# Kernel tuning notes

Hardware: AMD Instinct MI355X
Metric: run time of the kernel (lower is better)

## Reference

```python
import jax, jax.numpy as jnp
import numpy as np

B, S, HID, H = 2, 2048, 1024, 16
D_HEAD = HID // H  # 64
EPS = 1e-5


def _gammas():
    lo, hi = np.log(1.0 / 512.0), np.log(1.0 / 32.0)
    return (1.0 - np.exp(np.linspace(lo, hi, H))).astype(np.float32)


def _decay_mask():
    # D[h, n, m] = gamma_h^(n-m) for n >= m else 0  (causal exponential decay)
    gam = jnp.asarray(_gammas())                      # [H]
    pos = jnp.arange(S, dtype=jnp.float32)
    diff = pos[:, None] - pos[None, :]                # [S, S]
    keep = diff >= 0
    logg = jnp.log(gam)[:, None, None]                # [H,1,1]
    safe = jnp.where(keep, diff, 0.0)[None]           # avoid inf for masked entries
    return jnp.where(keep[None], jnp.exp(safe * logg), 0.0)  # [H, S, S]


def setup_inputs() -> dict:
    key = jax.random.key(0)
    ks = jax.random.split(key, 10)
    rn = lambda k, shape, s=1.0: jax.random.normal(k, shape, dtype=jnp.float32) * s
    return {
        "x": rn(ks[0], (B, S, HID)),
        "wq": rn(ks[1], (H, D_HEAD, D_HEAD), 1.0 / np.sqrt(D_HEAD)),
        "bq": rn(ks[2], (H, D_HEAD), 0.02),
        "wk": rn(ks[3], (H, D_HEAD, D_HEAD), 1.0 / np.sqrt(D_HEAD)),
        "bk": rn(ks[4], (H, D_HEAD), 0.02),
        "wv": rn(ks[5], (H, D_HEAD, D_HEAD), 1.0 / np.sqrt(D_HEAD)),
        "theta": rn(ks[6], (H, D_HEAD), 1.0 / D_HEAD),
        "gn_weight": jnp.ones((HID,), jnp.float32),
        "gn_bias": jnp.zeros((HID,), jnp.float32),
        "weight1": rn(ks[7], (HID, HID), 1.0 / HID),
        "weight2": rn(ks[8], (HID, HID), 1.0 / HID),
    }


def reference(x, wq, bq, wk, bk, wv, theta, gn_weight, gn_bias, weight1, weight2):
    # Per-head retention (all heads vectorized; torch loops over heads).
    xh = x.reshape(B, S, H, D_HEAD)
    q = jnp.einsum('bshd,hde->bshe', xh, wq) + bq
    k = jnp.einsum('bshd,hde->bshe', xh, wk) + bk
    v = jnp.einsum('bshd,hde->bshe', xh, wv)
    # Complex rotary factors exp(i*n*theta) on q, conj on k -> real part of q k^H:
    ang = jnp.arange(S, dtype=jnp.float32)[:, None, None] * theta[None]  # [S,H,d]
    cs, sn = jnp.cos(ang), jnp.sin(ang)
    scores = (jnp.einsum('bshd,bthd->bhst', q * cs, k * cs)
              + jnp.einsum('bshd,bthd->bhst', q * sn, k * sn))  # Re(QK^H) [B,H,S,S]
    scores = scores * _decay_mask()[None]                        # decay mask
    ret = jnp.einsum('bhst,bthd->bshd', scores, v)               # [B,S,H,d]
    # GroupNorm with groups = n_heads over channels (per-head normalization).
    mean = jnp.mean(ret, axis=-1, keepdims=True)
    var = jnp.var(ret, axis=-1, keepdims=True)
    retn = (ret - mean) * jax.lax.rsqrt(var + EPS)
    retn = retn.reshape(B, S, HID) * gn_weight + gn_bias
    # Swish gate on x @ W1, residual add, project with W2.
    gate = x @ weight1
    out = gate * jax.nn.sigmoid(gate) + retn
    return out @ weight2
```

## Files before the change

kernel.cpp:

```cpp
#include <hip/hip_runtime.h>
#include <cstdint>
#include <cstddef>

#define B_ 2
#define S_ 2048
#define HID_ 1024
#define H_ 16
#define DH_ 64

typedef __attribute__((ext_vector_type(8))) short short8;
typedef __attribute__((ext_vector_type(8))) unsigned short ushort8;
typedef __attribute__((ext_vector_type(4))) unsigned short ushort4v;
typedef __attribute__((ext_vector_type(4))) float floatx4;
typedef __attribute__((ext_vector_type(4))) float float4v;

static __device__ __forceinline__ unsigned short f2bf(float f) {
  unsigned int u = __float_as_uint(f);
  u += 0x7fffu + ((u >> 16) & 1u);
  return (unsigned short)(u >> 16);
}
static __device__ __forceinline__ float bf2f(unsigned short h) {
  return __uint_as_float(((unsigned int)h) << 16);
}

__global__ __launch_bounds__(256) void convert_kernel(
    const float* __restrict__ x, const float* __restrict__ w1,
    const float* __restrict__ w2, unsigned short* __restrict__ x_bf,
    unsigned short* __restrict__ w1t, unsigned short* __restrict__ w2t_hi,
    unsigned short* __restrict__ w2t_lo) {
  const int NX = B_ * S_ * HID_;
  const int NW = HID_ * HID_;
  int idx = blockIdx.x * 256 + threadIdx.x;
  if (idx < NX) {
    x_bf[idx] = f2bf(x[idx]);
  } else if (idx < NX + NW) {
    int i = idx - NX;
    int n = i >> 10, k = i & 1023;
    w1t[i] = f2bf(w1[k * HID_ + n]);
  } else if (idx < NX + 2 * NW) {
    int i = idx - NX - NW;
    int n = i >> 10, k = i & 1023;
    float v = w2[k * HID_ + n];
    unsigned short h = f2bf(v);
    w2t_hi[i] = h;
    w2t_lo[i] = f2bf(v - bf2f(h));
  }
}

__global__ __launch_bounds__(256) void qkv_kernel(
    const float* __restrict__ x, const float* __restrict__ wq,
    const float* __restrict__ bq, const float* __restrict__ wk,
    const float* __restrict__ bk, const float* __restrict__ wv,
    const float* __restrict__ theta,
    unsigned short* __restrict__ q_h, unsigned short* __restrict__ q_l,
    unsigned short* __restrict__ k_h, unsigned short* __restrict__ k_l,
    unsigned short* __restrict__ v_th, unsigned short* __restrict__ v_tl,
    int b) {
  __shared__ __align__(16) float xs[64 * 68];
  __shared__ __align__(16) float wqs[64 * 68];
  __shared__ __align__(16) float wks[64 * 68];
  __shared__ __align__(16) float wvs[64 * 68];

  int tid = threadIdx.x;
  int st = blockIdx.x, h = blockIdx.y;
  int s0 = st * 64;

#pragma unroll
  for (int i = 0; i < 4; ++i) {
    int cid = tid + i * 256;
    int r = cid >> 4, c4 = (cid & 15) * 4;
    *reinterpret_cast<float4v*>(&xs[r * 68 + c4]) =
        *reinterpret_cast<const float4v*>(x + ((size_t)(b * S_ + s0 + r)) * HID_ + h * DH_ + c4);
  }
#pragma unroll
  for (int i = 0; i < 4; ++i) {
    int cid = tid + i * 256;
    int d = cid >> 4, c4 = (cid & 15) * 4;
    *reinterpret_cast<float4v*>(&wqs[d * 68 + c4]) =
        *reinterpret_cast<const float4v*>(wq + (size_t)(h * DH_ + d) * DH_ + c4);
    *reinterpret_cast<float4v*>(&wks[d * 68 + c4]) =
        *reinterpret_cast<const float4v*>(wk + (size_t)(h * DH_ + d) * DH_ + c4);
    *reinterpret_cast<float4v*>(&wvs[d * 68 + c4]) =
        *reinterpret_cast<const float4v*>(wv + (size_t)(h * DH_ + d) * DH_ + c4);
  }
  __syncthreads();

  int rg = tid >> 3;
  int cg = tid & 7;
  int r0 = rg * 2, c0 = cg * 8;

  float aq[2][8], ak[2][8], av[2][8];
#pragma unroll
  for (int i = 0; i < 2; ++i)
#pragma unroll
    for (int j = 0; j < 8; ++j) { aq[i][j] = 0.f; ak[i][j] = 0.f; av[i][j] = 0.f; }

  for (int d = 0; d < 64; ++d) {
    float x0 = xs[(r0 + 0) * 68 + d];
    float x1 = xs[(r0 + 1) * 68 + d];
#pragma unroll
    for (int j = 0; j < 8; ++j) {
      float wqv = wqs[d * 68 + c0 + j];
      float wkv = wks[d * 68 + c0 + j];
      float wvv = wvs[d * 68 + c0 + j];
      aq[0][j] += x0 * wqv; aq[1][j] += x1 * wqv;
      ak[0][j] += x0 * wkv; ak[1][j] += x1 * wkv;
      av[0][j] += x0 * wvv; av[1][j] += x1 * wvv;
    }
  }

  float thv[8], bqv[8], bkv[8];
#pragma unroll
  for (int j = 0; j < 8; ++j) {
    thv[j] = theta[h * DH_ + c0 + j];
    bqv[j] = bq[h * DH_ + c0 + j];
    bkv[j] = bk[h * DH_ + c0 + j];
  }

  __syncthreads();
  unsigned short* VtH = reinterpret_cast<unsigned short*>(xs);
  unsigned short* VtL = reinterpret_cast<unsigned short*>(wqs);

#pragma unroll
  for (int i = 0; i < 2; ++i) {
    int s = s0 + r0 + i;
    size_t qb = ((size_t)h * S_ + s) * 128;
    ushort8 qch, qcl, qsh, qsl, kch, kcl, ksh, ksl;
#pragma unroll
    for (int j = 0; j < 8; ++j) {
      float q = aq[i][j] + bqv[j];
      float k = ak[i][j] + bkv[j];
      float ang = (float)s * thv[j];
      float cs = cosf(ang), sn = sinf(ang);
      float qc = q * cs, qs = q * sn;
      unsigned short hq1 = f2bf(qc);
      qch[j] = hq1;
      qcl[j] = f2bf(qc - bf2f(hq1));
      unsigned short hq2 = f2bf(qs);
      qsh[j] = hq2;
      qsl[j] = f2bf(qs - bf2f(hq2));
      float kc = k * cs, ksn = k * sn;
      unsigned short h1 = f2bf(kc);
      kch[j] = h1;
      kcl[j] = f2bf(kc - bf2f(h1));
      unsigned short h2 = f2bf(ksn);
      ksh[j] = h2;
      ksl[j] = f2bf(ksn - bf2f(h2));
      float vv = av[i][j];
      unsigned short vh1 = f2bf(vv);
      VtH[(c0 + j) * 72 + (r0 + i)] = vh1;
      VtL[(c0 + j) * 72 + (r0 + i)] = f2bf(vv - bf2f(vh1));
    }
    *reinterpret_cast<ushort8*>(q_h + qb + c0) = qch;
    *reinterpret_cast<ushort8*>(q_h + qb + 64 + c0) = qsh;
    *reinterpret_cast<ushort8*>(q_l + qb + c0) = qcl;
    *reinterpret_cast<ushort8*>(q_l + qb + 64 + c0) = qsl;
    *reinterpret_cast<ushort8*>(k_h + qb + c0) = kch;
    *reinterpret_cast<ushort8*>(k_h + qb + 64 + c0) = ksh;
    *reinterpret_cast<ushort8*>(k_l + qb + c0) = kcl;
    *reinterpret_cast<ushort8*>(k_l + qb + 64 + c0) = ksl;
  }
  __syncthreads();
#pragma unroll
  for (int i = 0; i < 2; ++i) {
    int cid = tid + i * 256;
    int d = cid >> 3, t8 = (cid & 7) * 8;
    size_t gb = ((size_t)(h * 64 + d)) * S_ + s0 + t8;
    *reinterpret_cast<ushort8*>(v_th + gb) = *reinterpret_cast<const ushort8*>(&VtH[d * 72 + t8]);
    *reinterpret_cast<ushort8*>(v_tl + gb) = *reinterpret_cast<const ushort8*>(&VtL[d * 72 + t8]);
  }
}

#define SCOFF(row, colb)   ((row) * 256 + ((colb) ^ (((row) & 7) << 4)))

__global__ __launch_bounds__(256, 2) void retention_split_kernel(
    const unsigned short* __restrict__ q_h, const unsigned short* __restrict__ q_l,
    const unsigned short* __restrict__ k_h, const unsigned short* __restrict__ k_l,
    const unsigned short* __restrict__ v_th, const unsigned short* __restrict__ v_tl,
    float* __restrict__ partial) {
  __shared__ __align__(16) unsigned short Kh[64 * 128];
  __shared__ __align__(16) unsigned short Kl[64 * 128];
  __shared__ __align__(16) unsigned short Vh[64 * 64];
  __shared__ __align__(16) unsigned short Vl[64 * 64];
  __shared__ __align__(16) float Sc[64 * 64];

  char* KhB = (char*)Kh;
  char* KlB = (char*)Kl;
  char* VhB = (char*)Vh;
  char* VlB = (char*)Vl;
  char* ScB = (char*)Sc;

  int tid = threadIdx.x;
  int w = tid >> 6;
  int lane = tid & 63, ln = lane & 15, quad = lane >> 4;
  int f = blockIdx.x;
  int h = ((f & 7) << 1) | ((f >> 3) & 1);
  int half = (f >> 4) & 1;
  int qt = 31 - (f >> 5);
  int s0 = qt * 64;
  int prow = quad * 4;

  int m = (qt + 2) >> 1;
  int kt0 = half ? m : 0;
  int kt1 = half ? (qt + 1) : m;

  const float lo_c = -6.2383246250395075f, hi_c = -3.4657359027997265f;
  float gam = 1.f - __expf(lo_c + (hi_c - lo_c) * ((float)h * (1.f / 15.f)));
  float logg = __logf(gam);

  float rowf[4], colf[4];
#pragma unroll
  for (int rr = 0; rr < 4; ++rr)
    rowf[rr] = __expf((float)(w * 16 + prow + rr) * logg);
#pragma unroll
  for (int ns = 0; ns < 4; ++ns)
    colf[ns] = __expf(-(float)(ns * 16 + ln) * logg);

  const unsigned short* khb = k_h + (size_t)h * S_ * 128;
  const unsigned short* klb = k_l + (size_t)h * S_ * 128;
  const unsigned short* vhb = v_th + (size_t)h * 64 * S_;
  const unsigned short* vlb = v_tl + (size_t)h * 64 * S_;

  int sQ = s0 + w * 16 + ln;
  const unsigned short* qhp = q_h + ((size_t)h * S_ + sQ) * 128 + quad * 8;
  const unsigned short* qlp = q_l + ((size_t)h * S_ + sQ) * 128 + quad * 8;
  short8 qfh[4], qfl[4];
#pragma unroll
  for (int c = 0; c < 4; ++c) {
    qfh[c] = *reinterpret_cast<const short8*>(qhp + c * 32);
    qfl[c] = *reinterpret_cast<const short8*>(qlp + c * 32);
  }

  floatx4 accO[4];
#pragma unroll
  for (int i = 0; i < 4; ++i) accO[i] = (floatx4){0.f, 0.f, 0.f, 0.f};

  ushort8 skh[4], skl[4], svh[2], svl[2];
  int t00 = kt0 * 64;
#pragma unroll
  for (int i = 0; i < 4; ++i) {
    int cid = tid + i * 256;
    int r = cid >> 4, c8 = (cid & 15) * 8;
    skh[i] = *reinterpret_cast<const ushort8*>(khb + ((size_t)(t00 + r)) * 128 + c8);
    skl[i] = *reinterpret_cast<const ushort8*>(klb + ((size_t)(t00 + r)) * 128 + c8);
  }
#pragma unroll
  for (int i = 0; i < 2; ++i) {
    int cid = tid + i * 256;
    int d = cid >> 3, t8 = (cid & 7) * 8;
    svh[i] = *reinterpret_cast<const ushort8*>(vhb + (size_t)d * S_ + t00 + t8);
    svl[i] = *reinterpret_cast<const ushort8*>(vlb + (size_t)d * S_ + t00 + t8);
  }
#pragma unroll
  for (int i = 0; i < 4; ++i) {
    int cid = tid + i * 256;
    int r = cid >> 4;
    int ko = r * 256 + (((cid & 15) * 16) ^ ((r & 7) << 4));
    *reinterpret_cast<ushort8*>(KhB + ko) = skh[i];
    *reinterpret_cast<ushort8*>(KlB + ko) = skl[i];
  }
#pragma unroll
  for (int i = 0; i < 2; ++i) {
    int cid = tid + i * 256;
    int d = cid >> 3;
    int vo = d * 128 + (((cid & 7) * 16) ^ ((d & 7) << 4));
    *reinterpret_cast<ushort8*>(VhB + vo) = svh[i];
    *reinterpret_cast<ushort8*>(VlB + vo) = svl[i];
  }
  if (kt0 + 1 < kt1) {
    int t01 = (kt0 + 1) * 64;
#pragma unroll
    for (int i = 0; i < 4; ++i) {
      int cid = tid + i * 256;
      int r = cid >> 4, c8 = (cid & 15) * 8;
      skh[i] = *reinterpret_cast<const ushort8*>(khb + ((size_t)(t01 + r)) * 128 + c8);
      skl[i] = *reinterpret_cast<const ushort8*>(klb + ((size_t)(t01 + r)) * 128 + c8);
    }
#pragma unroll
    for (int i = 0; i < 2; ++i) {
      int cid = tid + i * 256;
      int d = cid >> 3, t8 = (cid & 7) * 8;
      svh[i] = *reinterpret_cast<const ushort8*>(vhb + (size_t)d * S_ + t01 + t8);
      svl[i] = *reinterpret_cast<const ushort8*>(vlb + (size_t)d * S_ + t01 + t8);
    }
  }
  __syncthreads();

  for (int kt = kt0; kt < kt1; ++kt) {
    floatx4 accS[4];
#pragma unroll
    for (int ns = 0; ns < 4; ++ns) {
      floatx4 a = (floatx4){0.f, 0.f, 0.f, 0.f};
      int row = ns * 16 + ln;
#pragma unroll
      for (int ks = 0; ks < 4; ++ks) {
        int off = row * 256 + ((ks * 64 + quad * 16) ^ ((ln & 7) << 4));
        short8 kh = *reinterpret_cast<const short8*>(KhB + off);
        short8 kl = *reinterpret_cast<const short8*>(KlB + off);
        a = __builtin_amdgcn_mfma_f32_16x16x32_bf16(qfh[ks], kh, a, 0, 0, 0);
        a = __builtin_amdgcn_mfma_f32_16x16x32_bf16(qfl[ks], kh, a, 0, 0, 0);
        a = __builtin_amdgcn_mfma_f32_16x16x32_bf16(qfh[ks], kl, a, 0, 0, 0);
      }
      accS[ns] = a;
    }

    float tf = __expf((float)(64 * (qt - kt)) * logg);
    float trf[4];
#pragma unroll
    for (int rr = 0; rr < 4; ++rr) trf[rr] = tf * rowf[rr];
    if (kt < qt) {
#pragma unroll
      for (int ns = 0; ns < 4; ++ns) {
        int col = ns * 16 + ln;
#pragma unroll
        for (int rr = 0; rr < 4; ++rr) {
          int row = w * 16 + prow + rr;
          *reinterpret_cast<float*>(ScB + SCOFF(row, col * 4)) =
              accS[ns][rr] * trf[rr] * colf[ns];
        }
      }
    } else {
#pragma unroll
      for (int ns = 0; ns < 4; ++ns) {
        int col = ns * 16 + ln;
#pragma unroll
        for (int rr = 0; rr < 4; ++rr) {
          int row = w * 16 + prow + rr;
          float v = accS[ns][rr] * trf[rr] * colf[ns];
          *reinterpret_cast<float*>(ScB + SCOFF(row, col * 4)) =
              (row >= col) ? v : 0.f;
        }
      }
    }

#pragma unroll
    for (int ks = 0; ks < 2; ++ks) {
      int prw = w * 16 + ln;
      int cb = ks * 128 + quad * 32;
      float4v p0 = *reinterpret_cast<const float4v*>(ScB + SCOFF(prw, cb));
      float4v p1 = *reinterpret_cast<const float4v*>(ScB + SCOFF(prw, cb + 16));
      short8 ph, pl;
#pragma unroll
      for (int j = 0; j < 4; ++j) {
        unsigned short hh = f2bf(p0[j]);
        ph[j] = (short)hh;
        pl[j] = (short)f2bf(p0[j] - bf2f(hh));
        unsigned short hh2 = f2bf(p1[j]);
        ph[4 + j] = (short)hh2;
        pl[4 + j] = (short)f2bf(p1[j] - bf2f(hh2));
      }
#pragma unroll
      for (int ds = 0; ds < 4; ++ds) {
        int d = ds * 16 + ln;
        int voff = d * 128 + ((ks * 64 + quad * 16) ^ ((ln & 7) << 4));
        short8 vh = *reinterpret_cast<const short8*>(VhB + voff);
        short8 vl = *reinterpret_cast<const short8*>(VlB + voff);
        accO[ds] = __builtin_amdgcn_mfma_f32_16x16x32_bf16(ph, vh, accO[ds], 0, 0, 0);
        accO[ds] = __builtin_amdgcn_mfma_f32_16x16x32_bf16(pl, vh, accO[ds], 0, 0, 0);
        accO[ds] = __builtin_amdgcn_mfma_f32_16x16x32_bf16(ph, vl, accO[ds], 0, 0, 0);
      }
    }

    __syncthreads();
    if (kt + 1 < kt1) {
#pragma unroll
      for (int i = 0; i < 4; ++i) {
        int cid = tid + i * 256;
        int r = cid >> 4;
        int ko = r * 256 + (((cid & 15) * 16) ^ ((r & 7) << 4));
        *reinterpret_cast<ushort8*>(KhB + ko) = skh[i];
        *reinterpret_cast<ushort8*>(KlB + ko) = skl[i];
      }
#pragma unroll
      for (int i = 0; i < 2; ++i) {
        int cid = tid + i * 256;
        int d = cid >> 3;
        int vo = d * 128 + (((cid & 7) * 16) ^ ((d & 7) << 4));
        *reinterpret_cast<ushort8*>(VhB + vo) = svh[i];
        *reinterpret_cast<ushort8*>(VlB + vo) = svl[i];
      }
      if (kt + 2 < kt1) {
        int t0n = (kt + 2) * 64;
#pragma unroll
        for (int i = 0; i < 4; ++i) {
          int cid = tid + i * 256;
          int r = cid >> 4, c8 = (cid & 15) * 8;
          skh[i] = *reinterpret_cast<const ushort8*>(khb + ((size_t)(t0n + r)) * 128 + c8);
          skl[i] = *reinterpret_cast<const ushort8*>(klb + ((size_t)(t0n + r)) * 128 + c8);
        }
#pragma unroll
        for (int i = 0; i < 2; ++i) {
          int cid = tid + i * 256;
          int d = cid >> 3, t8 = (cid & 7) * 8;
          svh[i] = *reinterpret_cast<const ushort8*>(vhb + (size_t)d * S_ + t0n + t8);
          svl[i] = *reinterpret_cast<const ushort8*>(vlb + (size_t)d * S_ + t0n + t8);
        }
      }
      __syncthreads();
    }
  }

  float* pout = partial + ((size_t)(((h * 32 + qt) << 1) + half)) * 4096;
#pragma unroll
  for (int ds = 0; ds < 4; ++ds) {
#pragma unroll
    for (int rr = 0; rr < 4; ++rr) {
      pout[(w * 16 + quad * 4 + rr) * 64 + ds * 16 + ln] = accO[ds][rr];
    }
  }
}

__global__ __launch_bounds__(256) void combine_gn_kernel(
    const float* __restrict__ partial, const float* __restrict__ gn_w,
    const float* __restrict__ gn_b, float* __restrict__ retn, int b) {
  __shared__ float gnred[64][8];
  int tid = threadIdx.x;
  int qi = blockIdx.x;
  int h = qi >> 5, qt = qi & 31;
  const float* p0 = partial + (size_t)qi * 8192;
  const float* p1 = p0 + 4096;

  int r2 = tid >> 2;
  int sub = tid & 3;
  float a16[16];
#pragma unroll
  for (int c = 0; c < 4; ++c) {
    float4v va = *reinterpret_cast<const float4v*>(p0 + r2 * 64 + sub * 16 + c * 4);
    float4v vb = *reinterpret_cast<const float4v*>(p1 + r2 * 64 + sub * 16 + c * 4);
#pragma unroll
    for (int j = 0; j < 4; ++j) a16[c * 4 + j] = va[j] + vb[j];
  }

  float psum = 0.f, psq = 0.f;
#pragma unroll
  for (int i = 0; i < 16; ++i) { psum += a16[i]; psq += a16[i] * a16[i]; }
  gnred[r2][sub] = psum;
  gnred[r2][4 + sub] = psq;
  float sum = gnred[r2][0] + gnred[r2][1] + gnred[r2][2] + gnred[r2][3];
  float sq = gnred[r2][4] + gnred[r2][5] + gnred[r2][6] + gnred[r2][7];
  float mean = sum * (1.f / 64.f);
  float var = sq * (1.f / 64.f) - mean * mean;
  float rstd = rsqrtf(var + 1e-5f);

  size_t obase = ((size_t)(b * S_ + qt * 64 + r2)) * HID_ + h * DH_ + sub * 16;
#pragma unroll
  for (int i = 0; i < 16; ++i) {
    float gw = gn_w[h * DH_ + sub * 16 + i];
    float gb = gn_b[h * DH_ + sub * 16 + i];
    retn[obase + i] = (a16[i] - mean) * rstd * gw + gb;
  }
}

__global__ __launch_bounds__(256) void gemm_gate_kernel(
    const unsigned short* __restrict__ A, const unsigned short* __restrict__ Bt,
    const float* __restrict__ retn, unsigned short* __restrict__ pre_hi,
    unsigned short* __restrict__ pre_lo) {
  const int K = HID_;
  __shared__ __align__(16) unsigned short Al[128 * 56];
  __shared__ __align__(16) unsigned short Bl[128 * 56];

  int tid = threadIdx.x;
  int lane = tid & 63, ln = lane & 15, quad = lane >> 4;
  int w = tid >> 6, wm = w >> 1, wn = w & 1;
  int m0 = blockIdx.y * 128, n0 = blockIdx.x * 128;

  floatx4 acc[4][4];
#pragma unroll
  for (int i = 0; i < 4; ++i)
#pragma unroll
    for (int j = 0; j < 4; ++j) acc[i][j] = (floatx4){0.f, 0.f, 0.f, 0.f};

  for (int k0 = 0; k0 < K; k0 += 32) {
    __syncthreads();
#pragma unroll
    for (int i = 0; i < 2; ++i) {
      int cid = tid + i * 256;
      int r = cid >> 2, c8 = (cid & 3) * 8;
      *reinterpret_cast<ushort8*>(&Al[r * 56 + c8]) =
          *reinterpret_cast<const ushort8*>(A + (size_t)(m0 + r) * K + k0 + c8);
      *reinterpret_cast<ushort8*>(&Bl[r * 56 + c8]) =
          *reinterpret_cast<const ushort8*>(Bt + (size_t)(n0 + r) * K + k0 + c8);
    }
    __syncthreads();

    short8 af[4], bfr[4];
#pragma unroll
    for (int i = 0; i < 4; ++i) {
      af[i] = *reinterpret_cast<const short8*>(&Al[(wm * 64 + i * 16 + ln) * 56 + quad * 8]);
      bfr[i] = *reinterpret_cast<const short8*>(&Bl[(wn * 64 + i * 16 + ln) * 56 + quad * 8]);
    }
#pragma unroll
    for (int mi = 0; mi < 4; ++mi)
#pragma unroll
      for (int ni = 0; ni < 4; ++ni)
        acc[mi][ni] = __builtin_amdgcn_mfma_f32_16x16x32_bf16(af[mi], bfr[ni], acc[mi][ni], 0, 0, 0);
  }

#pragma unroll
  for (int mi = 0; mi < 4; ++mi) {
#pragma unroll
    for (int r = 0; r < 4; ++r) {
      int row = m0 + wm * 64 + mi * 16 + quad * 4 + r;
#pragma unroll
      for (int ni = 0; ni < 4; ++ni) {
        int col = n0 + wn * 64 + ni * 16 + ln;
        float g = acc[mi][ni][r];
        float val = g * (1.f / (1.f + __expf(-g))) + retn[(size_t)row * HID_ + col];
        unsigned short hh = f2bf(val);
        size_t oidx = (size_t)row * HID_ + col;
        pre_hi[oidx] = hh;
        pre_lo[oidx] = f2bf(val - bf2f(hh));
      }
    }
  }
}

__global__ __launch_bounds__(256) void gemm_out_kernel(
    const unsigned short* __restrict__ Ah, const unsigned short* __restrict__ Alo,
    const unsigned short* __restrict__ Bth, const unsigned short* __restrict__ Btlo,
    float* __restrict__ out_f) {
  const int K = HID_;
  __shared__ __align__(16) unsigned short AhS[128 * 56];
  __shared__ __align__(16) unsigned short AlS[128 * 56];
  __shared__ __align__(16) unsigned short BhS[128 * 56];
  __shared__ __align__(16) unsigned short BlS[128 * 56];

  int tid = threadIdx.x;
  int lane = tid & 63, ln = lane & 15, quad = lane >> 4;
  int w = tid >> 6, wm = w >> 1, wn = w & 1;
  int m0 = blockIdx.y * 128, n0 = blockIdx.x * 128;

  floatx4 acc[4][4];
#pragma unroll
  for (int i = 0; i < 4; ++i)
#pragma unroll
    for (int j = 0; j < 4; ++j) acc[i][j] = (floatx4){0.f, 0.f, 0.f, 0.f};

  for (int k0 = 0; k0 < K; k0 += 32) {
    __syncthreads();
#pragma unroll
    for (int i = 0; i < 2; ++i) {
      int cid = tid + i * 256;
      int r = cid >> 2, c8 = (cid & 3) * 8;
      size_t ga = (size_t)(m0 + r) * K + k0 + c8;
      size_t gb = (size_t)(n0 + r) * K + k0 + c8;
      *reinterpret_cast<ushort8*>(&AhS[r * 56 + c8]) = *reinterpret_cast<const ushort8*>(Ah + ga);
      *reinterpret_cast<ushort8*>(&AlS[r * 56 + c8]) = *reinterpret_cast<const ushort8*>(Alo + ga);
      *reinterpret_cast<ushort8*>(&BhS[r * 56 + c8]) = *reinterpret_cast<const ushort8*>(Bth + gb);
      *reinterpret_cast<ushort8*>(&BlS[r * 56 + c8]) = *reinterpret_cast<const ushort8*>(Btlo + gb);
    }
    __syncthreads();

    short8 afh[4], afl[4], bfh[4], bfl[4];
#pragma unroll
    for (int i = 0; i < 4; ++i) {
      int ao = (wm * 64 + i * 16 + ln) * 56 + quad * 8;
      int bo = (wn * 64 + i * 16 + ln) * 56 + quad * 8;
      afh[i] = *reinterpret_cast<const short8*>(&AhS[ao]);
      afl[i] = *reinterpret_cast<const short8*>(&AlS[ao]);
      bfh[i] = *reinterpret_cast<const short8*>(&BhS[bo]);
      bfl[i] = *reinterpret_cast<const short8*>(&BlS[bo]);
    }
#pragma unroll
    for (int mi = 0; mi < 4; ++mi)
#pragma unroll
      for (int ni = 0; ni < 4; ++ni) {
        floatx4 a = acc[mi][ni];
        a = __builtin_amdgcn_mfma_f32_16x16x32_bf16(afh[mi], bfh[ni], a, 0, 0, 0);
        a = __builtin_amdgcn_mfma_f32_16x16x32_bf16(afl[mi], bfh[ni], a, 0, 0, 0);
        a = __builtin_amdgcn_mfma_f32_16x16x32_bf16(afh[mi], bfl[ni], a, 0, 0, 0);
        acc[mi][ni] = a;
      }
  }

#pragma unroll
  for (int mi = 0; mi < 4; ++mi) {
#pragma unroll
    for (int r = 0; r < 4; ++r) {
      int row = m0 + wm * 64 + mi * 16 + quad * 4 + r;
#pragma unroll
      for (int ni = 0; ni < 4; ++ni) {
        int col = n0 + wn * 64 + ni * 16 + ln;
        out_f[(size_t)row * HID_ + col] = acc[mi][ni][r];
      }
    }
  }
}

extern "C" void kernel_launch(void* const* d_in, const int* in_sizes, int n_in,
                              void* d_out, int out_size, void* d_ws,
                              size_t ws_size, hipStream_t stream) {
  (void)in_sizes; (void)n_in; (void)out_size; (void)ws_size;
  const float* x = (const float*)d_in[0];
  const float* wq = (const float*)d_in[1];
  const float* bq = (const float*)d_in[2];
  const float* wk = (const float*)d_in[3];
  const float* bk = (const float*)d_in[4];
  const float* wv = (const float*)d_in[5];
  const float* theta = (const float*)d_in[6];
  const float* gn_w = (const float*)d_in[7];
  const float* gn_b = (const float*)d_in[8];
  const float* w1 = (const float*)d_in[9];
  const float* w2 = (const float*)d_in[10];

  const size_t MB = 1024 * 1024;
  char* ws = (char*)d_ws;
  unsigned short* x_bf   = (unsigned short*)(ws + 0 * MB);
  unsigned short* w1t    = (unsigned short*)(ws + 8 * MB);
  unsigned short* w2t_hi = (unsigned short*)(ws + 10 * MB);
  unsigned short* w2t_lo = (unsigned short*)(ws + 12 * MB);
  unsigned short* q_h    = (unsigned short*)(ws + 14 * MB);
  unsigned short* q_l    = (unsigned short*)(ws + 22 * MB);
  unsigned short* k_h    = (unsigned short*)(ws + 30 * MB);
  unsigned short* k_l    = (unsigned short*)(ws + 38 * MB);
  unsigned short* v_th   = (unsigned short*)(ws + 46 * MB);
  unsigned short* v_tl   = (unsigned short*)(ws + 50 * MB);
  float*          retn   = (float*)(ws + 54 * MB);
  float*          partial= (float*)(ws + 70 * MB);
  unsigned short* pre_hi = (unsigned short*)(ws + 14 * MB);
  unsigned short* pre_lo = (unsigned short*)(ws + 22 * MB);
  float* out = (float*)d_out;

  convert_kernel<<<dim3(24576), 256, 0, stream>>>(x, w1, w2, x_bf, w1t, w2t_hi, w2t_lo);
  for (int b = 0; b < B_; ++b) {
    qkv_kernel<<<dim3(S_ / 64, H_), 256, 0, stream>>>(
        x, wq, bq, wk, bk, wv, theta, q_h, q_l, k_h, k_l, v_th, v_tl, b);
    retention_split_kernel<<<dim3(1024), 256, 0, stream>>>(
        q_h, q_l, k_h, k_l, v_th, v_tl, partial);
    combine_gn_kernel<<<dim3(512), 256, 0, stream>>>(
        partial, gn_w, gn_b, retn, b);
  }
  gemm_gate_kernel<<<dim3(HID_ / 128, (B_ * S_) / 128), 256, 0, stream>>>(
      x_bf, w1t, retn, pre_hi, pre_lo);
  gemm_out_kernel<<<dim3(HID_ / 128, (B_ * S_) / 128), 256, 0, stream>>>(
      pre_hi, pre_lo, w2t_hi, w2t_lo, out);
}
```

Before: 345.4 us.

## Retile retention QK^T as 2x2 warp grid and halve GEMM N-tiles

The retention kernel's score computation now tiles 64x64 scores as a 2x2 warp grid, so each warp computes 32x32 and reuses each K fragment load across two Q row tiles. This cuts LDS reads of K per MFMA, at the cost of more Q fragment registers and an extra block barrier before the PV stage. The launch-bounds occupancy hint is dropped. The gate and output GEMMs shrink their N tile from 128 to 64, doubling the grid to 512 blocks to fill more CUs, at the cost of less reuse of the A tile.

```diff
diff --git a/kernel.cpp b/kernel.cpp
--- a/kernel.cpp
+++ b/kernel.cpp
@@ -173,7 +173,7 @@
 
 #define SCOFF(row, colb)   ((row) * 256 + ((colb) ^ (((row) & 7) << 4)))
 
-__global__ __launch_bounds__(256, 2) void retention_split_kernel(
+__global__ __launch_bounds__(256) void retention_split_kernel(
     const unsigned short* __restrict__ q_h, const unsigned short* __restrict__ q_l,
     const unsigned short* __restrict__ k_h, const unsigned short* __restrict__ k_l,
     const unsigned short* __restrict__ v_th, const unsigned short* __restrict__ v_tl,
@@ -193,12 +193,12 @@
   int tid = threadIdx.x;
   int w = tid >> 6;
   int lane = tid & 63, ln = lane & 15, quad = lane >> 4;
+  int wr = w >> 1, wc = w & 1;
   int f = blockIdx.x;
   int h = ((f & 7) << 1) | ((f >> 3) & 1);
   int half = (f >> 4) & 1;
   int qt = 31 - (f >> 5);
   int s0 = qt * 64;
-  int prow = quad * 4;
 
   int m = (qt + 2) >> 1;
   int kt0 = half ? m : 0;
@@ -208,27 +208,32 @@
   float gam = 1.f - __expf(lo_c + (hi_c - lo_c) * ((float)h * (1.f / 15.f)));
   float logg = __logf(gam);
 
-  float rowf[4], colf[4];
-#pragma unroll
-  for (int rr = 0; rr < 4; ++rr)
-    rowf[rr] = __expf((float)(w * 16 + prow + rr) * logg);
-#pragma unroll
-  for (int ns = 0; ns < 4; ++ns)
-    colf[ns] = __expf(-(float)(ns * 16 + ln) * logg);
+  float rowf[2][4], colf[2];
+#pragma unroll
+  for (int rt = 0; rt < 2; ++rt)
+#pragma unroll
+    for (int rr = 0; rr < 4; ++rr)
+      rowf[rt][rr] = __expf((float)(wr * 32 + rt * 16 + quad * 4 + rr) * logg);
+#pragma unroll
+  for (int ns = 0; ns < 2; ++ns)
+    colf[ns] = __expf(-(float)(wc * 32 + ns * 16 + ln) * logg);
 
   const unsigned short* khb = k_h + (size_t)h * S_ * 128;
   const unsigned short* klb = k_l + (size_t)h * S_ * 128;
   const unsigned short* vhb = v_th + (size_t)h * 64 * S_;
   const unsigned short* vlb = v_tl + (size_t)h * 64 * S_;
 
-  int sQ = s0 + w * 16 + ln;
-  const unsigned short* qhp = q_h + ((size_t)h * S_ + sQ) * 128 + quad * 8;
-  const unsigned short* qlp = q_l + ((size_t)h * S_ + sQ) * 128 + quad * 8;
-  short8 qfh[4], qfl[4];
-#pragma unroll
-  for (int c = 0; c < 4; ++c) {
-    qfh[c] = *reinterpret_cast<const short8*>(qhp + c * 32);
-    qfl[c] = *reinterpret_cast<const short8*>(qlp + c * 32);
+  short8 qfh[2][4], qfl[2][4];
+#pragma unroll
+  for (int rt = 0; rt < 2; ++rt) {
+    int sQ = s0 + wr * 32 + rt * 16 + ln;
+    const unsigned short* qhp = q_h + ((size_t)h * S_ + sQ) * 128 + quad * 8;
+    const unsigned short* qlp = q_l + ((size_t)h * S_ + sQ) * 128 + quad * 8;
+#pragma unroll
+    for (int c = 0; c < 4; ++c) {
+      qfh[rt][c] = *reinterpret_cast<const short8*>(qhp + c * 32);
+      qfl[rt][c] = *reinterpret_cast<const short8*>(qlp + c * 32);
+    }
   }
 
   floatx4 accO[4];
@@ -236,102 +241,116 @@
   for (int i = 0; i < 4; ++i) accO[i] = (floatx4){0.f, 0.f, 0.f, 0.f};
 
   ushort8 skh[4], skl[4], svh[2], svl[2];
-  int t00 = kt0 * 64;
-#pragma unroll
-  for (int i = 0; i < 4; ++i) {
-    int cid = tid + i * 256;
-    int r = cid >> 4, c8 = (cid & 15) * 8;
-    skh[i] = *reinterpret_cast<const ushort8*>(khb + ((size_t)(t00 + r)) * 128 + c8);
-    skl[i] = *reinterpret_cast<const ushort8*>(klb + ((size_t)(t00 + r)) * 128 + c8);
-  }
-#pragma unroll
-  for (int i = 0; i < 2; ++i) {
-    int cid = tid + i * 256;
-    int d = cid >> 3, t8 = (cid & 7) * 8;
-    svh[i] = *reinterpret_cast<const ushort8*>(vhb + (size_t)d * S_ + t00 + t8);
-    svl[i] = *reinterpret_cast<const ushort8*>(vlb + (size_t)d * S_ + t00 + t8);
-  }
-#pragma unroll
-  for (int i = 0; i < 4; ++i) {
-    int cid = tid + i * 256;
-    int r = cid >> 4;
-    int ko = r * 256 + (((cid & 15) * 16) ^ ((r & 7) << 4));
-    *reinterpret_cast<ushort8*>(KhB + ko) = skh[i];
-    *reinterpret_cast<ushort8*>(KlB + ko) = skl[i];
-  }
-#pragma unroll
-  for (int i = 0; i < 2; ++i) {
-    int cid = tid + i * 256;
-    int d = cid >> 3;
-    int vo = d * 128 + (((cid & 7) * 16) ^ ((d & 7) << 4));
-    *reinterpret_cast<ushort8*>(VhB + vo) = svh[i];
-    *reinterpret_cast<ushort8*>(VlB + vo) = svl[i];
-  }
-  if (kt0 + 1 < kt1) {
-    int t01 = (kt0 + 1) * 64;
+  {
+    int t00 = kt0 * 64;
 #pragma unroll
     for (int i = 0; i < 4; ++i) {
       int cid = tid + i * 256;
       int r = cid >> 4, c8 = (cid & 15) * 8;
-      skh[i] = *reinterpret_cast<const ushort8*>(khb + ((size_t)(t01 + r)) * 128 + c8);
-      skl[i] = *reinterpret_cast<const ushort8*>(klb + ((size_t)(t01 + r)) * 128 + c8);
+      skh[i] = *reinterpret_cast<const ushort8*>(khb + ((size_t)(t00 + r)) * 128 + c8);
+      skl[i] = *reinterpret_cast<const ushort8*>(klb + ((size_t)(t00 + r)) * 128 + c8);
     }
 #pragma unroll
     for (int i = 0; i < 2; ++i) {
       int cid = tid + i * 256;
       int d = cid >> 3, t8 = (cid & 7) * 8;
-      svh[i] = *reinterpret_cast<const ushort8*>(vhb + (size_t)d * S_ + t01 + t8);
-      svl[i] = *reinterpret_cast<const ushort8*>(vlb + (size_t)d * S_ + t01 + t8);
+      svh[i] = *reinterpret_cast<const ushort8*>(vhb + (size_t)d * S_ + t00 + t8);
+      svl[i] = *reinterpret_cast<const ushort8*>(vlb + (size_t)d * S_ + t00 + t8);
+    }
+#pragma unroll
+    for (int i = 0; i < 4; ++i) {
+      int cid = tid + i * 256;
+      int r = cid >> 4;
+      int ko = r * 256 + (((cid & 15) * 16) ^ ((r & 7) << 4));
+      *reinterpret_cast<ushort8*>(KhB + ko) = skh[i];
+      *reinterpret_cast<ushort8*>(KlB + ko) = skl[i];
+    }
+#pragma unroll
+    for (int i = 0; i < 2; ++i) {
+      int cid = tid + i * 256;
+      int d = cid >> 3;
+      int vo = d * 128 + (((cid & 7) * 16) ^ ((d & 7) << 4));
+      *reinterpret_cast<ushort8*>(VhB + vo) = svh[i];
+      *reinterpret_cast<ushort8*>(VlB + vo) = svl[i];
+    }
+    if (kt0 + 1 < kt1) {
+      int t01 = (kt0 + 1) * 64;
+#pragma unroll
+      for (int i = 0; i < 4; ++i) {
+        int cid = tid + i * 256;
+        int r = cid >> 4, c8 = (cid & 15) * 8;
+        skh[i] = *reinterpret_cast<const ushort8*>(khb + ((size_t)(t01 + r)) * 128 + c8);
+        skl[i] = *reinterpret_cast<const ushort8*>(klb + ((size_t)(t01 + r)) * 128 + c8);
+      }
+#pragma unroll
+      for (int i = 0; i < 2; ++i) {
+        int cid = tid + i * 256;
+        int d = cid >> 3, t8 = (cid & 7) * 8;
+        svh[i] = *reinterpret_cast<const ushort8*>(vhb + (size_t)d * S_ + t01 + t8);
+        svl[i] = *reinterpret_cast<const ushort8*>(vlb + (size_t)d * S_ + t01 + t8);
+      }
     }
   }
   __syncthreads();
 
   for (int kt = kt0; kt < kt1; ++kt) {
-    floatx4 accS[4];
-#pragma unroll
-    for (int ns = 0; ns < 4; ++ns) {
-      floatx4 a = (floatx4){0.f, 0.f, 0.f, 0.f};
-      int row = ns * 16 + ln;
+    floatx4 accS[2][2];
+#pragma unroll
+    for (int rt = 0; rt < 2; ++rt)
+#pragma unroll
+      for (int ns = 0; ns < 2; ++ns) accS[rt][ns] = (floatx4){0.f, 0.f, 0.f, 0.f};
+#pragma unroll
+    for (int ns = 0; ns < 2; ++ns) {
+      int krow = wc * 32 + ns * 16 + ln;
 #pragma unroll
       for (int ks = 0; ks < 4; ++ks) {
-        int off = row * 256 + ((ks * 64 + quad * 16) ^ ((ln & 7) << 4));
+        int off = krow * 256 + ((ks * 64 + quad * 16) ^ ((ln & 7) << 4));
         short8 kh = *reinterpret_cast<const short8*>(KhB + off);
         short8 kl = *reinterpret_cast<const short8*>(KlB + off);
-        a = __builtin_amdgcn_mfma_f32_16x16x32_bf16(qfh[ks], kh, a, 0, 0, 0);
-        a = __builtin_amdgcn_mfma_f32_16x16x32_bf16(qfl[ks], kh, a, 0, 0, 0);
-        a = __builtin_amdgcn_mfma_f32_16x16x32_bf16(qfh[ks], kl, a, 0, 0, 0);
-      }
-      accS[ns] = a;
+#pragma unroll
+        for (int rt = 0; rt < 2; ++rt) {
+          accS[rt][ns] = __builtin_amdgcn_mfma_f32_16x16x32_bf16(qfh[rt][ks], kh, accS[rt][ns], 0, 0, 0);
+          accS[rt][ns] = __builtin_amdgcn_mfma_f32_16x16x32_bf16(qfl[rt][ks], kh, accS[rt][ns], 0, 0, 0);
+          accS[rt][ns] = __builtin_amdgcn_mfma_f32_16x16x32_bf16(qfh[rt][ks], kl, accS[rt][ns], 0, 0, 0);
+        }
+      }
     }
 
     float tf = __expf((float)(64 * (qt - kt)) * logg);
-    float trf[4];
-#pragma unroll
-    for (int rr = 0; rr < 4; ++rr) trf[rr] = tf * rowf[rr];
+    float trf[2][4];
+#pragma unroll
+    for (int rt = 0; rt < 2; ++rt)
+#pragma unroll
+      for (int rr = 0; rr < 4; ++rr) trf[rt][rr] = tf * rowf[rt][rr];
     if (kt < qt) {
 #pragma unroll
-      for (int ns = 0; ns < 4; ++ns) {
-        int col = ns * 16 + ln;
-#pragma unroll
-        for (int rr = 0; rr < 4; ++rr) {
-          int row = w * 16 + prow + rr;
-          *reinterpret_cast<float*>(ScB + SCOFF(row, col * 4)) =
-              accS[ns][rr] * trf[rr] * colf[ns];
+      for (int rt = 0; rt < 2; ++rt)
+#pragma unroll
+        for (int ns = 0; ns < 2; ++ns) {
+          int col = wc * 32 + ns * 16 + ln;
+#pragma unroll
+          for (int rr = 0; rr < 4; ++rr) {
+            int row = wr * 32 + rt * 16 + quad * 4 + rr;
+            *reinterpret_cast<float*>(ScB + SCOFF(row, col * 4)) =
+                accS[rt][ns][rr] * trf[rt][rr] * colf[ns];
+          }
         }
-      }
     } else {
 #pragma unroll
-      for (int ns = 0; ns < 4; ++ns) {
-        int col = ns * 16 + ln;
-#pragma unroll
-        for (int rr = 0; rr < 4; ++rr) {
-          int row = w * 16 + prow + rr;
-          float v = accS[ns][rr] * trf[rr] * colf[ns];
-          *reinterpret_cast<float*>(ScB + SCOFF(row, col * 4)) =
-              (row >= col) ? v : 0.f;
+      for (int rt = 0; rt < 2; ++rt)
+#pragma unroll
+        for (int ns = 0; ns < 2; ++ns) {
+          int col = wc * 32 + ns * 16 + ln;
+#pragma unroll
+          for (int rr = 0; rr < 4; ++rr) {
+            int row = wr * 32 + rt * 16 + quad * 4 + rr;
+            float v = accS[rt][ns][rr] * trf[rt][rr] * colf[ns];
+            *reinterpret_cast<float*>(ScB + SCOFF(row, col * 4)) =
+                (row >= col) ? v : 0.f;
+          }
         }
-      }
-    }
+    }
+    __syncthreads();
 
 #pragma unroll
     for (int ks = 0; ks < 2; ++ks) {
@@ -425,8 +444,9 @@
   float a16[16];
 #pragma unroll
   for (int c = 0; c < 4; ++c) {
-    float4v va = *reinterpret_cast<const float4v*>(p0 + r2 * 64 + sub * 16 + c * 4);
-    float4v vb = *reinterpret_cast<const float4v*>(p1 + r2 * 64 + sub * 16 + c * 4);
+    int o = r2 * 64 + sub * 16 + c * 4;
+    float4v va = *reinterpret_cast<const float4v*>(p0 + o);
+    float4v vb = *reinterpret_cast<const float4v*>(p1 + o);
 #pragma unroll
     for (int j = 0; j < 4; ++j) a16[c * 4 + j] = va[j] + vb[j];
   }
@@ -457,18 +477,18 @@
     unsigned short* __restrict__ pre_lo) {
   const int K = HID_;
   __shared__ __align__(16) unsigned short Al[128 * 56];
-  __shared__ __align__(16) unsigned short Bl[128 * 56];
+  __shared__ __align__(16) unsigned short Bl[64 * 56];
 
   int tid = threadIdx.x;
   int lane = tid & 63, ln = lane & 15, quad = lane >> 4;
   int w = tid >> 6, wm = w >> 1, wn = w & 1;
-  int m0 = blockIdx.y * 128, n0 = blockIdx.x * 128;
-
-  floatx4 acc[4][4];
+  int m0 = blockIdx.y * 128, n0 = blockIdx.x * 64;
+
+  floatx4 acc[4][2];
 #pragma unroll
   for (int i = 0; i < 4; ++i)
 #pragma unroll
-    for (int j = 0; j < 4; ++j) acc[i][j] = (floatx4){0.f, 0.f, 0.f, 0.f};
+    for (int j = 0; j < 2; ++j) acc[i][j] = (floatx4){0.f, 0.f, 0.f, 0.f};
 
   for (int k0 = 0; k0 < K; k0 += 32) {
     __syncthreads();
@@ -478,21 +498,25 @@
       int r = cid >> 2, c8 = (cid & 3) * 8;
       *reinterpret_cast<ushort8*>(&Al[r * 56 + c8]) =
           *reinterpret_cast<const ushort8*>(A + (size_t)(m0 + r) * K + k0 + c8);
+    }
+    {
+      int r = tid >> 2, c8 = (tid & 3) * 8;
       *reinterpret_cast<ushort8*>(&Bl[r * 56 + c8]) =
           *reinterpret_cast<const ushort8*>(Bt + (size_t)(n0 + r) * K + k0 + c8);
     }
     __syncthreads();
 
-    short8 af[4], bfr[4];
-#pragma unroll
-    for (int i = 0; i < 4; ++i) {
+    short8 af[4], bfr[2];
+#pragma unroll
+    for (int i = 0; i < 4; ++i)
       af[i] = *reinterpret_cast<const short8*>(&Al[(wm * 64 + i * 16 + ln) * 56 + quad * 8]);
-      bfr[i] = *reinterpret_cast<const short8*>(&Bl[(wn * 64 + i * 16 + ln) * 56 + quad * 8]);
-    }
+#pragma unroll
+    for (int i = 0; i < 2; ++i)
+      bfr[i] = *reinterpret_cast<const short8*>(&Bl[(wn * 32 + i * 16 + ln) * 56 + quad * 8]);
 #pragma unroll
     for (int mi = 0; mi < 4; ++mi)
 #pragma unroll
-      for (int ni = 0; ni < 4; ++ni)
+      for (int ni = 0; ni < 2; ++ni)
         acc[mi][ni] = __builtin_amdgcn_mfma_f32_16x16x32_bf16(af[mi], bfr[ni], acc[mi][ni], 0, 0, 0);
   }
 
@@ -502,8 +526,8 @@
     for (int r = 0; r < 4; ++r) {
       int row = m0 + wm * 64 + mi * 16 + quad * 4 + r;
 #pragma unroll
-      for (int ni = 0; ni < 4; ++ni) {
-        int col = n0 + wn * 64 + ni * 16 + ln;
+      for (int ni = 0; ni < 2; ++ni) {
+        int col = n0 + wn * 32 + ni * 16 + ln;
         float g = acc[mi][ni][r];
         float val = g * (1.f / (1.f + __expf(-g))) + retn[(size_t)row * HID_ + col];
         unsigned short hh = f2bf(val);
@@ -522,19 +546,19 @@
   const int K = HID_;
   __shared__ __align__(16) unsigned short AhS[128 * 56];
   __shared__ __align__(16) unsigned short AlS[128 * 56];
-  __shared__ __align__(16) unsigned short BhS[128 * 56];
-  __shared__ __align__(16) unsigned short BlS[128 * 56];
+  __shared__ __align__(16) unsigned short BhS[64 * 56];
+  __shared__ __align__(16) unsigned short BlS[64 * 56];
 
   int tid = threadIdx.x;
   int lane = tid & 63, ln = lane & 15, quad = lane >> 4;
   int w = tid >> 6, wm = w >> 1, wn = w & 1;
-  int m0 = blockIdx.y * 128, n0 = blockIdx.x * 128;
-
-  floatx4 acc[4][4];
+  int m0 = blockIdx.y * 128, n0 = blockIdx.x * 64;
+
+  floatx4 acc[4][2];
 #pragma unroll
   for (int i = 0; i < 4; ++i)
 #pragma unroll
-    for (int j = 0; j < 4; ++j) acc[i][j] = (floatx4){0.f, 0.f, 0.f, 0.f};
+    for (int j = 0; j < 2; ++j) acc[i][j] = (floatx4){0.f, 0.f, 0.f, 0.f};
 
   for (int k0 = 0; k0 < K; k0 += 32) {
     __syncthreads();
@@ -543,28 +567,34 @@
       int cid = tid + i * 256;
       int r = cid >> 2, c8 = (cid & 3) * 8;
       size_t ga = (size_t)(m0 + r) * K + k0 + c8;
-      size_t gb = (size_t)(n0 + r) * K + k0 + c8;
       *reinterpret_cast<ushort8*>(&AhS[r * 56 + c8]) = *reinterpret_cast<const ushort8*>(Ah + ga);
       *reinterpret_cast<ushort8*>(&AlS[r * 56 + c8]) = *reinterpret_cast<const ushort8*>(Alo + ga);
+    }
+    {
+      int r = tid >> 2, c8 = (tid & 3) * 8;
+      size_t gb = (size_t)(n0 + r) * K + k0 + c8;
       *reinterpret_cast<ushort8*>(&BhS[r * 56 + c8]) = *reinterpret_cast<const ushort8*>(Bth + gb);
       *reinterpret_cast<ushort8*>(&BlS[r * 56 + c8]) = *reinterpret_cast<const ushort8*>(Btlo + gb);
     }
     __syncthreads();
 
-    short8 afh[4], afl[4], bfh[4], bfl[4];
+    short8 afh[4], afl[4], bfh[2], bfl[2];
 #pragma unroll
     for (int i = 0; i < 4; ++i) {
       int ao = (wm * 64 + i * 16 + ln) * 56 + quad * 8;
-      int bo = (wn * 64 + i * 16 + ln) * 56 + quad * 8;
       afh[i] = *reinterpret_cast<const short8*>(&AhS[ao]);
       afl[i] = *reinterpret_cast<const short8*>(&AlS[ao]);
+    }
+#pragma unroll
+    for (int i = 0; i < 2; ++i) {
+      int bo = (wn * 32 + i * 16 + ln) * 56 + quad * 8;
       bfh[i] = *reinterpret_cast<const short8*>(&BhS[bo]);
       bfl[i] = *reinterpret_cast<const short8*>(&BlS[bo]);
     }
 #pragma unroll
     for (int mi = 0; mi < 4; ++mi)
 #pragma unroll
-      for (int ni = 0; ni < 4; ++ni) {
+      for (int ni = 0; ni < 2; ++ni) {
         floatx4 a = acc[mi][ni];
         a = __builtin_amdgcn_mfma_f32_16x16x32_bf16(afh[mi], bfh[ni], a, 0, 0, 0);
         a = __builtin_amdgcn_mfma_f32_16x16x32_bf16(afl[mi], bfh[ni], a, 0, 0, 0);
@@ -579,8 +609,8 @@
     for (int r = 0; r < 4; ++r) {
       int row = m0 + wm * 64 + mi * 16 + quad * 4 + r;
 #pragma unroll
-      for (int ni = 0; ni < 4; ++ni) {
-        int col = n0 + wn * 64 + ni * 16 + ln;
+      for (int ni = 0; ni < 2; ++ni) {
+        int col = n0 + wn * 32 + ni * 16 + ln;
         out_f[(size_t)row * HID_ + col] = acc[mi][ni][r];
       }
     }
@@ -630,8 +660,8 @@
     combine_gn_kernel<<<dim3(512), 256, 0, stream>>>(
         partial, gn_w, gn_b, retn, b);
   }
-  gemm_gate_kernel<<<dim3(HID_ / 128, (B_ * S_) / 128), 256, 0, stream>>>(
+  gemm_gate_kernel<<<dim3(HID_ / 64, (B_ * S_) / 128), 256, 0, stream>>>(
       x_bf, w1t, retn, pre_hi, pre_lo);
-  gemm_out_kernel<<<dim3(HID_ / 128, (B_ * S_) / 128), 256, 0, stream>>>(
+  gemm_out_kernel<<<dim3(HID_ / 64, (B_ * S_) / 128), 256, 0, stream>>>(
       pre_hi, pre_lo, w2t_hi, w2t_lo, out);
 }
```

Result: faster. 338.0 us (-2.2%).
